# Kernel optimization log

Measured on AMD Instinct MI355X. Metric: run time of the kernel, lower is better.

Reference implementation:

```python
import jax, jax.numpy as jnp
import numpy as np

N_NODES = 50000
N_EDGES = 800000
IN_C, HID_C, OUT_C = 64, 128, 40


def setup_inputs() -> dict:
    key = jax.random.key(0)
    ks = jax.random.split(key, 8)
    x = jax.random.normal(ks[0], (N_NODES, IN_C), dtype=jnp.float32)
    edge_index = jax.random.randint(ks[1], (2, N_EDGES), 0, N_NODES, dtype=jnp.int64)
    def lin(k, fan_in, fan_out):
        # torch Linear default init: U(-1/sqrt(fan_in), 1/sqrt(fan_in))
        bound = 1.0 / np.sqrt(fan_in)
        kw, kb = jax.random.split(k)
        w = jax.random.uniform(kw, (fan_in, fan_out), minval=-bound, maxval=bound, dtype=jnp.float32)
        b = jax.random.uniform(kb, (fan_out,), minval=-bound, maxval=bound, dtype=jnp.float32)
        return w, b
    w1a, b1a = lin(ks[2], IN_C, HID_C)
    w1b, b1b = lin(ks[3], HID_C, HID_C)
    w2a, b2a = lin(ks[4], HID_C, HID_C)
    w2b, b2b = lin(ks[5], HID_C, OUT_C)
    return {
        'x': x, 'edge_index': edge_index,
        'w1a': w1a, 'b1a': b1a, 'w1b': w1b, 'b1b': b1b, 'eps1': jnp.float32(0.0),
        'w2a': w2a, 'b2a': b2a, 'w2b': w2b, 'b2b': b2b, 'eps2': jnp.float32(0.0),
    }


def _gin_conv(x, src, dst, eps, wa, ba, wb, bb):
    # aggregate: sum of neighbor (source) features at each destination node
    agg = jax.ops.segment_sum(x[src], dst, num_segments=N_NODES)  # [N, d]
    h = (1.0 + eps) * x + agg
    h = jax.nn.relu(h @ wa + ba)
    return h @ wb + bb


def reference(x, edge_index, w1a, b1a, w1b, b1b, eps1, w2a, b2a, w2b, b2b, eps2):
    src, dst = edge_index[0], edge_index[1]
    h = _gin_conv(x, src, dst, eps1, w1a, b1a, w1b, b1b)
    h = jax.nn.relu(h)
    # F.dropout(training=False) -> identity at inference
    h = _gin_conv(h, src, dst, eps2, w2a, b2a, w2b, b2b)
    return jax.nn.log_softmax(h, axis=1)
```

## Files before the change

kernel.cpp:

```cpp
#include <hip/hip_runtime.h>
#include <math.h>

#define N_NODES 50000
#define N_EDGES 800000
#define DUMMY   50000

typedef __attribute__((ext_vector_type(4))) _Float16 half4;
typedef __attribute__((ext_vector_type(8))) _Float16 half8;
typedef __attribute__((ext_vector_type(4))) float f32x4;

__global__ __launch_bounds__(256) void convert_zero(const float4* __restrict__ in,
    half4* __restrict__ xh4, int* __restrict__ zbase, half4* __restrict__ h1dummy)
{
    int i = blockIdx.x * 256 + threadIdx.x;
    if (i < 450000) zbase[i] = 0;
    if (i < 800000) {
        float4 v = in[i];
        half4 h;
        h[0] = (_Float16)v.x; h[1] = (_Float16)v.y;
        h[2] = (_Float16)v.z; h[3] = (_Float16)v.w;
        xh4[i] = h;
    } else if (i < 800016) {
        half4 zer = {(_Float16)0.f, (_Float16)0.f, (_Float16)0.f, (_Float16)0.f};
        xh4[i] = zer;
    }
    if (i < 32) {
        half4 zer = {(_Float16)0.f, (_Float16)0.f, (_Float16)0.f, (_Float16)0.f};
        h1dummy[i] = zer;
    }
}

__global__ __launch_bounds__(256) void scatter_ell(const int* __restrict__ src,
    const int* __restrict__ dst, int* __restrict__ cursor8, int* __restrict__ ovcur,
    unsigned short* __restrict__ ellp, unsigned short* __restrict__ ovell)
{
    int g = blockIdx.x & 7;
    int el = (blockIdx.x >> 3) * 256 + threadIdx.x;
    if (el >= 100000) return;
    int e = g * 100000 + el;
    int d = dst[e];
    unsigned short s = (unsigned short)src[e];
    int slot = atomicAdd(&cursor8[g * 50000 + d], 1);
    if (slot < 8) ellp[(size_t)(g * 50000 + d) * 8 + slot] = s;
    else {
        int o = atomicAdd(&ovcur[d], 1);
        if (o < 16) ovell[d * 16 + o] = s;
    }
}

__global__ __launch_bounds__(256) void gather64c(const half8* __restrict__ rows,
    const int* __restrict__ cursor8, const int* __restrict__ ovcur,
    const unsigned short* __restrict__ ellp, const unsigned short* __restrict__ ovell,
    unsigned short* __restrict__ ell, int* __restrict__ deg,
    const float* __restrict__ epsp, half8* __restrict__ z)
{
    __shared__ unsigned short buf[4][80];
    const float eps = 1.0f + epsp[0];
    const int lane = threadIdx.x & 63;
    const int w = threadIdx.x >> 6;
    const int q = lane & 7, p = lane >> 3;
    const int sl = lane & 7;
    const int wid = blockIdx.x * 4 + w;
    const int wstep = gridDim.x * 4;

    for (int node = wid; node < N_NODES; node += wstep) {
        int cg = min(cursor8[p * 50000 + node], 8);
        bool valid = sl < cg;
        unsigned short v = ellp[(size_t)(p * 50000 + node) * 8 + sl];
        unsigned long long mask = __ballot(valid);
        int total = __popcll(mask);
        int pos = __popcll(mask & ((1ULL << lane) - 1ULL));
        if (valid) buf[w][pos] = v;
        int ov = min(ovcur[node], 16);
        if (lane < ov) buf[w][total + lane] = ovell[node * 16 + lane];
        int tot = min(total + ov, 64);
        unsigned short e = (lane < tot) ? buf[w][lane] : (unsigned short)DUMMY;
        ell[((size_t)node << 6) + lane] = e;
        if (lane == 0) deg[node] = tot;
        int eidx = e;
        float acc[8];
        #pragma unroll
        for (int j = 0; j < 8; ++j) acc[j] = 0.f;
        for (int i = 0; i < tot; i += 32) {
            int s0 = __shfl(eidx, i + p);
            int s1 = __shfl(eidx, i + 8 + p);
            int s2 = __shfl(eidx, i + 16 + p);
            int s3 = __shfl(eidx, i + 24 + p);
            half8 v0 = rows[s0 * 8 + q];
            half8 v1 = rows[s1 * 8 + q];
            half8 v2 = rows[s2 * 8 + q];
            half8 v3 = rows[s3 * 8 + q];
            #pragma unroll
            for (int j = 0; j < 8; ++j)
                acc[j] += ((float)v0[j] + (float)v1[j]) + ((float)v2[j] + (float)v3[j]);
        }
        #pragma unroll
        for (int j = 0; j < 8; ++j) {
            acc[j] += __shfl_xor(acc[j], 8);
            acc[j] += __shfl_xor(acc[j], 16);
            acc[j] += __shfl_xor(acc[j], 32);
        }
        if (p == 0) {
            half8 sv = rows[node * 8 + q];
            half8 o;
            #pragma unroll
            for (int j = 0; j < 8; ++j) o[j] = (_Float16)fmaf(eps, (float)sv[j], acc[j]);
            z[node * 8 + q] = o;
        }
    }
}

__global__ __launch_bounds__(256) void gather128(const half8* __restrict__ rows,
    const unsigned short* __restrict__ ell, const int* __restrict__ deg,
    const float* __restrict__ epsp, half8* __restrict__ z)
{
    const float eps = 1.0f + epsp[0];
    const int lane = threadIdx.x & 63;
    const int q = lane & 15, p = lane >> 4;
    const int wid = blockIdx.x * 4 + (threadIdx.x >> 6);
    const int wstep = gridDim.x * 4;

    for (int node = wid; node < N_NODES; node += wstep) {
        const int cnt = deg[node];
        int eidx = ell[((size_t)node << 6) + lane];
        float acc[8];
        #pragma unroll
        for (int j = 0; j < 8; ++j) acc[j] = 0.f;
        for (int i = 0; i < cnt; i += 16) {
            int s0 = __shfl(eidx, i + p);
            int s1 = __shfl(eidx, i + 4 + p);
            int s2 = __shfl(eidx, i + 8 + p);
            int s3 = __shfl(eidx, i + 12 + p);
            half8 v0 = rows[s0 * 16 + q];
            half8 v1 = rows[s1 * 16 + q];
            half8 v2 = rows[s2 * 16 + q];
            half8 v3 = rows[s3 * 16 + q];
            #pragma unroll
            for (int j = 0; j < 8; ++j)
                acc[j] += ((float)v0[j] + (float)v1[j]) + ((float)v2[j] + (float)v3[j]);
        }
        #pragma unroll
        for (int j = 0; j < 8; ++j) {
            acc[j] += __shfl_xor(acc[j], 16);
            acc[j] += __shfl_xor(acc[j], 32);
        }
        if (p == 0) {
            half8 sv = rows[node * 16 + q];
            half8 o;
            #pragma unroll
            for (int j = 0; j < 8; ++j) o[j] = (_Float16)fmaf(eps, (float)sv[j], acc[j]);
            z[node * 16 + q] = o;
        }
    }
}

template<int KA, int NB, int EPI>
__global__ __launch_bounds__(512) void fused_mlp(const _Float16* __restrict__ A,
    const float* __restrict__ wA, const float* __restrict__ bA,
    const float* __restrict__ wB, const float* __restrict__ bB,
    void* __restrict__ Cout, int NwB)
{
    constexpr int SA = KA / 32, CTB = NB / 16;
    extern __shared__ char smem[];
    half8* fragA = (half8*)smem;
    half8* fragB = (half8*)(smem + SA * 8 * 2 * 64 * 16);
    char* midbase = smem + SA * 8 * 2 * 64 * 16 + 4 * CTB * 2 * 64 * 16;
    const int tid = threadIdx.x;

    for (int idx = tid; idx < SA * 8 * 64; idx += 512) {
        int l = idx & 63, f = idx >> 6;
        int s = f >> 3, ct = f & 7;
        int c = ct * 16 + (l & 15);
        int k0 = s * 32 + (l >> 4) * 8;
        half8 hi, lo;
        #pragma unroll
        for (int i = 0; i < 8; ++i) {
            float wv = wA[(k0 + i) * 128 + c];
            _Float16 h = (_Float16)wv;
            hi[i] = h;
            lo[i] = (_Float16)(wv - (float)h);
        }
        fragA[(f * 2 + 0) * 64 + l] = hi;
        fragA[(f * 2 + 1) * 64 + l] = lo;
    }
    for (int idx = tid; idx < 4 * CTB * 64; idx += 512) {
        int l = idx & 63, f = idx >> 6;
        int s = f / CTB, ct = f % CTB;
        int c = ct * 16 + (l & 15);
        int k0 = s * 32 + (l >> 4) * 8;
        half8 hi, lo;
        #pragma unroll
        for (int i = 0; i < 8; ++i) {
            float wv = (c < NwB) ? wB[(k0 + i) * NwB + c] : 0.0f;
            _Float16 h = (_Float16)wv;
            hi[i] = h;
            lo[i] = (_Float16)(wv - (float)h);
        }
        fragB[(f * 2 + 0) * 64 + l] = hi;
        fragB[(f * 2 + 1) * 64 + l] = lo;
    }
    __syncthreads();

    const int lane = tid & 63;
    const int gg = lane >> 4, r16 = lane & 15;
    const int tile = blockIdx.x * 8 + (tid >> 6);
    if (tile >= N_NODES / 16) return;
    char* my = midbase + (tid >> 6) * 4096;

    const _Float16* Ar = A + (size_t)(tile * 16 + r16) * KA;
    f32x4 acc[8];
    #pragma unroll
    for (int ct = 0; ct < 8; ++ct) acc[ct] = (f32x4){0.f, 0.f, 0.f, 0.f};
    #pragma unroll
    for (int s = 0; s < SA; ++s) {
        half8 a = *(const half8*)(Ar + s * 32 + gg * 8);
        #pragma unroll
        for (int ct = 0; ct < 8; ++ct) {
            half8 bh = fragA[((s * 8 + ct) * 2 + 0) * 64 + lane];
            half8 bo = fragA[((s * 8 + ct) * 2 + 1) * 64 + lane];
            acc[ct] = __builtin_amdgcn_mfma_f32_16x16x32_f16(a, bh, acc[ct], 0, 0, 0);
            acc[ct] = __builtin_amdgcn_mfma_f32_16x16x32_f16(a, bo, acc[ct], 0, 0, 0);
        }
    }
    #pragma unroll
    for (int ct = 0; ct < 8; ++ct) {
        float bb = bA[ct * 16 + r16];
        #pragma unroll
        for (int r = 0; r < 4; ++r) {
            int row = gg * 4 + r;
            float v = fmaxf(acc[ct][r] + bb, 0.0f);
            int off = (row << 8) + ((ct * 16 + r16) << 1);
            off ^= (row & 7) << 4;
            *(_Float16*)(my + off) = (_Float16)v;
        }
    }

    half8 a2[4];
    #pragma unroll
    for (int s = 0; s < 4; ++s) {
        int off = (r16 << 8) + (s << 6) + (gg << 4);
        off ^= (r16 & 7) << 4;
        a2[s] = *(const half8*)(my + off);
    }
    f32x4 acc2[CTB];
    #pragma unroll
    for (int ct = 0; ct < CTB; ++ct) acc2[ct] = (f32x4){0.f, 0.f, 0.f, 0.f};
    #pragma unroll
    for (int s = 0; s < 4; ++s) {
        #pragma unroll
        for (int ct = 0; ct < CTB; ++ct) {
            half8 bh = fragB[((s * CTB + ct) * 2 + 0) * 64 + lane];
            half8 bo = fragB[((s * CTB + ct) * 2 + 1) * 64 + lane];
            acc2[ct] = __builtin_amdgcn_mfma_f32_16x16x32_f16(a2[s], bh, acc2[ct], 0, 0, 0);
            acc2[ct] = __builtin_amdgcn_mfma_f32_16x16x32_f16(a2[s], bo, acc2[ct], 0, 0, 0);
        }
    }

    if (EPI == 0) {
        _Float16* C = (_Float16*)Cout;
        #pragma unroll
        for (int ct = 0; ct < CTB; ++ct) {
            float bb = bB[ct * 16 + r16];
            #pragma unroll
            for (int r = 0; r < 4; ++r) {
                int row = tile * 16 + gg * 4 + r;
                float v = fmaxf(acc2[ct][r] + bb, 0.0f);
                C[(size_t)row * NB + ct * 16 + r16] = (_Float16)v;
            }
        }
    } else {
        float* C = (float*)Cout;
        const bool va2 = r16 < 8;
        float bl0 = bB[r16], bl1 = bB[16 + r16];
        float bl2 = va2 ? bB[32 + r16] : 0.0f;
        #pragma unroll
        for (int r = 0; r < 4; ++r) {
            int row = tile * 16 + gg * 4 + r;
            float v0 = acc2[0][r] + bl0;
            float v1 = acc2[1][r] + bl1;
            float v2 = acc2[2][r] + bl2;
            float mx = fmaxf(fmaxf(v0, v1), va2 ? v2 : -__builtin_inff());
            mx = fmaxf(mx, __shfl_xor(mx, 1));
            mx = fmaxf(mx, __shfl_xor(mx, 2));
            mx = fmaxf(mx, __shfl_xor(mx, 4));
            mx = fmaxf(mx, __shfl_xor(mx, 8));
            float sm = expf(v0 - mx) + expf(v1 - mx) + (va2 ? expf(v2 - mx) : 0.f);
            sm += __shfl_xor(sm, 1);
            sm += __shfl_xor(sm, 2);
            sm += __shfl_xor(sm, 4);
            sm += __shfl_xor(sm, 8);
            float ls = logf(sm) + mx;
            C[row * 40 + r16] = v0 - ls;
            C[row * 40 + 16 + r16] = v1 - ls;
            if (va2) C[row * 40 + 32 + r16] = v2 - ls;
        }
    }
}

extern "C" void kernel_launch(void* const* d_in, const int* in_sizes, int n_in,
                              void* d_out, int out_size, void* d_ws, size_t ws_size,
                              hipStream_t stream) {
    const float* x    = (const float*)d_in[0];
    const int*   ei   = (const int*)d_in[1];
    const float* w1a  = (const float*)d_in[2];
    const float* b1a  = (const float*)d_in[3];
    const float* w1b  = (const float*)d_in[4];
    const float* b1b  = (const float*)d_in[5];
    const float* eps1 = (const float*)d_in[6];
    const float* w2a  = (const float*)d_in[7];
    const float* b2a  = (const float*)d_in[8];
    const float* w2b  = (const float*)d_in[9];
    const float* b2b  = (const float*)d_in[10];
    const float* eps2 = (const float*)d_in[11];
    float* out = (float*)d_out;

    const int* srcIdx = ei;
    const int* dstIdx = ei + N_EDGES;

    char* ws = (char*)d_ws;
    int*            cursor8 = (int*)(ws);
    int*            ovcur   = (int*)(ws + 1600000);
    unsigned short* ellp    = (unsigned short*)(ws + 1800000);
    unsigned short* ovell   = (unsigned short*)(ws + 8200000);
    unsigned short* ell     = (unsigned short*)(ws + 9800000);
    int*            deg     = (int*)(ws + 16200000);
    _Float16*       xh      = (_Float16*)(ws + 16400000);
    _Float16*       z1h     = (_Float16*)(ws + 22800128);
    _Float16*       h1h     = (_Float16*)(ws + 29200128);
    _Float16*       z2h     = (_Float16*)(ws + 42000384);
    half4*          h1dummy = (half4*)(h1h + (size_t)DUMMY * 128);

    convert_zero<<<3126, 256, 0, stream>>>((const float4*)x, (half4*)xh, cursor8, h1dummy);
    scatter_ell<<<3128, 256, 0, stream>>>(srcIdx, dstIdx, cursor8, ovcur, ellp, ovell);

    gather64c<<<2048, 256, 0, stream>>>((const half8*)xh, cursor8, ovcur, ellp, ovell,
                                        ell, deg, eps1, (half8*)z1h);
    fused_mlp<64, 128, 0><<<391, 512, 131072, stream>>>(z1h, w1a, b1a, w1b, b1b, h1h, 128);
    gather128<<<2048, 256, 0, stream>>>((const half8*)h1h, ell, deg, eps2, (half8*)z2h);
    fused_mlp<128, 48, 1><<<391, 512, 122880, stream>>>(z2h, w2a, b2a, w2b, b2b, out, 40);
}
```

Measured before the change: 207.6 us.

## Precompute split-fp16 weight fragments once and read them from global in MLP kernels

Result: slower. 212.1 us (+2.1%).

```diff
diff --git a/kernel.cpp b/kernel.cpp
--- a/kernel.cpp
+++ b/kernel.cpp
@@ -9,8 +9,16 @@
 typedef __attribute__((ext_vector_type(8))) _Float16 half8;
 typedef __attribute__((ext_vector_type(4))) float f32x4;
 
-__global__ __launch_bounds__(256) void convert_zero(const float4* __restrict__ in,
-    half4* __restrict__ xh4, int* __restrict__ zbase, half4* __restrict__ h1dummy)
+#define F_W1A 0
+#define F_W1B (16 * 128)
+#define F_W2A (48 * 128)
+#define F_W2B (80 * 128)
+
+__global__ __launch_bounds__(256) void prep(const float4* __restrict__ in,
+    half4* __restrict__ xh4, int* __restrict__ zbase, half4* __restrict__ h1dummy,
+    const float* __restrict__ w1a, const float* __restrict__ w1b,
+    const float* __restrict__ w2a, const float* __restrict__ w2b,
+    half8* __restrict__ wfrag)
 {
     int i = blockIdx.x * 256 + threadIdx.x;
     if (i < 450000) zbase[i] = 0;
@@ -27,6 +35,27 @@
     if (i < 32) {
         half4 zer = {(_Float16)0.f, (_Float16)0.f, (_Float16)0.f, (_Float16)0.f};
         h1dummy[i] = zer;
+    }
+    int j = i - 800032;
+    if (j >= 0 && j < 5888) {
+        int l = j & 63, f = j >> 6;
+        const float* W; int fi, s, ct, Nw, base;
+        if (f < 16)      { W = w1a; fi = f;      s = fi >> 3; ct = fi & 7;    Nw = 128; base = F_W1A; }
+        else if (f < 48) { W = w1b; fi = f - 16; s = fi >> 3; ct = fi & 7;    Nw = 128; base = F_W1B; }
+        else if (f < 80) { W = w2a; fi = f - 48; s = fi >> 3; ct = fi & 7;    Nw = 128; base = F_W2A; }
+        else             { W = w2b; fi = f - 80; s = fi / 3;  ct = fi - s*3;  Nw = 40;  base = F_W2B; }
+        int c = ct * 16 + (l & 15);
+        int k0 = s * 32 + (l >> 4) * 8;
+        half8 hi, lo;
+        #pragma unroll
+        for (int t = 0; t < 8; ++t) {
+            float wv = (c < Nw) ? W[(k0 + t) * Nw + c] : 0.0f;
+            _Float16 h = (_Float16)wv;
+            hi[t] = h;
+            lo[t] = (_Float16)(wv - (float)h);
+        }
+        wfrag[base + (fi * 2 + 0) * 64 + l] = hi;
+        wfrag[base + (fi * 2 + 1) * 64 + l] = lo;
     }
 }
 
@@ -155,57 +184,20 @@
 }
 
 template<int KA, int NB, int EPI>
-__global__ __launch_bounds__(512) void fused_mlp(const _Float16* __restrict__ A,
-    const float* __restrict__ wA, const float* __restrict__ bA,
-    const float* __restrict__ wB, const float* __restrict__ bB,
-    void* __restrict__ Cout, int NwB)
+__global__ __launch_bounds__(256) void fused_mlp(const _Float16* __restrict__ A,
+    const half8* __restrict__ wAF, const float* __restrict__ bA,
+    const half8* __restrict__ wBF, const float* __restrict__ bB,
+    void* __restrict__ Cout)
 {
     constexpr int SA = KA / 32, CTB = NB / 16;
-    extern __shared__ char smem[];
-    half8* fragA = (half8*)smem;
-    half8* fragB = (half8*)(smem + SA * 8 * 2 * 64 * 16);
-    char* midbase = smem + SA * 8 * 2 * 64 * 16 + 4 * CTB * 2 * 64 * 16;
+    __shared__ char mid[4][4096];
     const int tid = threadIdx.x;
-
-    for (int idx = tid; idx < SA * 8 * 64; idx += 512) {
-        int l = idx & 63, f = idx >> 6;
-        int s = f >> 3, ct = f & 7;
-        int c = ct * 16 + (l & 15);
-        int k0 = s * 32 + (l >> 4) * 8;
-        half8 hi, lo;
-        #pragma unroll
-        for (int i = 0; i < 8; ++i) {
-            float wv = wA[(k0 + i) * 128 + c];
-            _Float16 h = (_Float16)wv;
-            hi[i] = h;
-            lo[i] = (_Float16)(wv - (float)h);
-        }
-        fragA[(f * 2 + 0) * 64 + l] = hi;
-        fragA[(f * 2 + 1) * 64 + l] = lo;
-    }
-    for (int idx = tid; idx < 4 * CTB * 64; idx += 512) {
-        int l = idx & 63, f = idx >> 6;
-        int s = f / CTB, ct = f % CTB;
-        int c = ct * 16 + (l & 15);
-        int k0 = s * 32 + (l >> 4) * 8;
-        half8 hi, lo;
-        #pragma unroll
-        for (int i = 0; i < 8; ++i) {
-            float wv = (c < NwB) ? wB[(k0 + i) * NwB + c] : 0.0f;
-            _Float16 h = (_Float16)wv;
-            hi[i] = h;
-            lo[i] = (_Float16)(wv - (float)h);
-        }
-        fragB[(f * 2 + 0) * 64 + l] = hi;
-        fragB[(f * 2 + 1) * 64 + l] = lo;
-    }
-    __syncthreads();
-
     const int lane = tid & 63;
+    const int wave = tid >> 6;
     const int gg = lane >> 4, r16 = lane & 15;
-    const int tile = blockIdx.x * 8 + (tid >> 6);
-    if (tile >= N_NODES / 16) return;
-    char* my = midbase + (tid >> 6) * 4096;
+    const int tile = blockIdx.x * 4 + wave;
+    if (tile >= (N_NODES + 15) / 16) return;
+    char* my = mid[wave];
 
     const _Float16* Ar = A + (size_t)(tile * 16 + r16) * KA;
     f32x4 acc[8];
@@ -216,8 +208,8 @@
         half8 a = *(const half8*)(Ar + s * 32 + gg * 8);
         #pragma unroll
         for (int ct = 0; ct < 8; ++ct) {
-            half8 bh = fragA[((s * 8 + ct) * 2 + 0) * 64 + lane];
-            half8 bo = fragA[((s * 8 + ct) * 2 + 1) * 64 + lane];
+            half8 bh = wAF[((s * 8 + ct) * 2 + 0) * 64 + lane];
+            half8 bo = wAF[((s * 8 + ct) * 2 + 1) * 64 + lane];
             acc[ct] = __builtin_amdgcn_mfma_f32_16x16x32_f16(a, bh, acc[ct], 0, 0, 0);
             acc[ct] = __builtin_amdgcn_mfma_f32_16x16x32_f16(a, bo, acc[ct], 0, 0, 0);
         }
@@ -249,8 +241,8 @@
     for (int s = 0; s < 4; ++s) {
         #pragma unroll
         for (int ct = 0; ct < CTB; ++ct) {
-            half8 bh = fragB[((s * CTB + ct) * 2 + 0) * 64 + lane];
-            half8 bo = fragB[((s * CTB + ct) * 2 + 1) * 64 + lane];
+            half8 bh = wBF[((s * CTB + ct) * 2 + 0) * 64 + lane];
+            half8 bo = wBF[((s * CTB + ct) * 2 + 1) * 64 + lane];
             acc2[ct] = __builtin_amdgcn_mfma_f32_16x16x32_f16(a2[s], bh, acc2[ct], 0, 0, 0);
             acc2[ct] = __builtin_amdgcn_mfma_f32_16x16x32_f16(a2[s], bo, acc2[ct], 0, 0, 0);
         }
@@ -324,18 +316,22 @@
     unsigned short* ovell   = (unsigned short*)(ws + 8200000);
     unsigned short* ell     = (unsigned short*)(ws + 9800000);
     int*            deg     = (int*)(ws + 16200000);
-    _Float16*       xh      = (_Float16*)(ws + 16400000);
-    _Float16*       z1h     = (_Float16*)(ws + 22800128);
-    _Float16*       h1h     = (_Float16*)(ws + 29200128);
-    _Float16*       z2h     = (_Float16*)(ws + 42000384);
+    half8*          wfrag   = (half8*)(ws + 16400000);
+    _Float16*       xh      = (_Float16*)(ws + 16600000);
+    _Float16*       z1h     = (_Float16*)(ws + 23000192);
+    _Float16*       h1h     = (_Float16*)(ws + 29400192);
+    _Float16*       z2h     = (_Float16*)(ws + 42200448);
     half4*          h1dummy = (half4*)(h1h + (size_t)DUMMY * 128);
 
-    convert_zero<<<3126, 256, 0, stream>>>((const float4*)x, (half4*)xh, cursor8, h1dummy);
+    prep<<<3149, 256, 0, stream>>>((const float4*)x, (half4*)xh, cursor8, h1dummy,
+                                   w1a, w1b, w2a, w2b, wfrag);
     scatter_ell<<<3128, 256, 0, stream>>>(srcIdx, dstIdx, cursor8, ovcur, ellp, ovell);
 
     gather64c<<<2048, 256, 0, stream>>>((const half8*)xh, cursor8, ovcur, ellp, ovell,
                                         ell, deg, eps1, (half8*)z1h);
-    fused_mlp<64, 128, 0><<<391, 512, 131072, stream>>>(z1h, w1a, b1a, w1b, b1b, h1h, 128);
+    fused_mlp<64, 128, 0><<<782, 256, 0, stream>>>(z1h, wfrag + F_W1A, b1a,
+                                                   wfrag + F_W1B, b1b, h1h);
     gather128<<<2048, 256, 0, stream>>>((const half8*)h1h, ell, deg, eps2, (half8*)z2h);
-    fused_mlp<128, 48, 1><<<391, 512, 122880, stream>>>(z2h, w2a, b2a, w2b, b2b, out, 40);
-}
+    fused_mlp<128, 48, 1><<<782, 256, 0, stream>>>(z2h, wfrag + F_W2A, b2a,
+                                                   wfrag + F_W2B, b2b, out);
+}
```
